# Optimization experiments

Hardware: AMD Instinct MI355X
Metric: run time of the kernel (lower is better)

## Reference

```python
import jax, jax.numpy as jnp
import numpy as np
from jax.scipy.linalg import solve_triangular

B, D, NL, NH, DH = 16, 768, 12, 12, 64
P, S, LP, NC = 10, 5, 5, 100
IMG, PATCH = 224, 16
NPTOK = (IMG // PATCH) ** 2  # 196 patches
DFF = 4 * D
LOG2PI = float(np.log(2.0 * np.pi))


def setup_inputs() -> dict:
    key = jax.random.key(0)
    ks = jax.random.split(key, 12)
    s = 0.02
    inp = {}
    inp['inputs'] = jax.random.normal(ks[0], (B, 3, IMG, IMG), jnp.float32)
    inp['patch_w'] = jax.random.normal(ks[1], (D, 3, PATCH, PATCH), jnp.float32) * s
    inp['patch_b'] = jnp.zeros((D,), jnp.float32)
    inp['cls_token'] = jax.random.normal(ks[2], (1, 1, D), jnp.float32) * s
    inp['pos_embed'] = jax.random.normal(ks[3], (1, NPTOK + 1, D), jnp.float32) * s
    inp['ln1_g'] = jnp.ones((NL, D), jnp.float32)
    inp['ln1_b'] = jnp.zeros((NL, D), jnp.float32)
    inp['qkv_w'] = jax.random.normal(ks[4], (NL, D, 3 * D), jnp.float32) * s
    inp['qkv_b'] = jnp.zeros((NL, 3 * D), jnp.float32)
    inp['proj_w'] = jax.random.normal(ks[5], (NL, D, D), jnp.float32) * s
    inp['proj_b'] = jnp.zeros((NL, D), jnp.float32)
    inp['ln2_g'] = jnp.ones((NL, D), jnp.float32)
    inp['ln2_b'] = jnp.zeros((NL, D), jnp.float32)
    inp['fc1_w'] = jax.random.normal(ks[6], (NL, D, DFF), jnp.float32) * s
    inp['fc1_b'] = jnp.zeros((NL, DFF), jnp.float32)
    inp['fc2_w'] = jax.random.normal(ks[7], (NL, DFF, D), jnp.float32) * s
    inp['fc2_b'] = jnp.zeros((NL, D), jnp.float32)
    inp['norm_g'] = jnp.ones((D,), jnp.float32)
    inp['norm_b'] = jnp.zeros((D,), jnp.float32)
    inp['head_w'] = jax.random.normal(ks[8], (D, NC), jnp.float32) * s
    inp['head_b'] = jnp.zeros((NC,), jnp.float32)
    inp['prompt'] = jax.random.normal(ks[9], (P, LP, D), jnp.float32)
    m = jax.random.normal(ks[10], (P, D), jnp.float32)
    inp['mean'] = m / jnp.linalg.norm(m, axis=-1, keepdims=True)
    # init in torch: ones + eye, repeated per pool component (positive definite)
    inp['variance'] = jnp.ones((P, D, D), jnp.float32) + jnp.eye(D, dtype=jnp.float32)[None]
    return inp


def _ln(x, g, b, eps=1e-6):
    m = x.mean(-1, keepdims=True)
    v = jnp.mean((x - m) ** 2, axis=-1, keepdims=True)
    return (x - m) * jax.lax.rsqrt(v + eps) * g + b


def _blocks(x, blk):
    def step(x, pl):
        g1, b1, qw, qb, pw, pb, g2, b2, f1w, f1b, f2w, f2b = pl
        Bn, N, _ = x.shape
        h = _ln(x, g1, b1)
        qkv = (h @ qw + qb).reshape(Bn, N, 3, NH, DH).transpose(2, 0, 3, 1, 4)
        q, k, v = qkv[0], qkv[1], qkv[2]  # [B,H,N,dh]
        att = jax.nn.softmax(jnp.einsum('bhqd,bhkd->bhqk', q, k) * (1.0 / np.sqrt(DH)), axis=-1)
        o = jnp.einsum('bhqk,bhkd->bhqd', att, v).transpose(0, 2, 1, 3).reshape(Bn, N, D)
        x = x + o @ pw + pb
        h = _ln(x, g2, b2)
        return x + jax.nn.gelu(h @ f1w + f1b) @ f2w + f2b, None
    x, _ = jax.lax.scan(step, x, blk)
    return x


def _mvn_logprob(q, mean, cov):
    # q: [B,D]; mean: [P,D]; cov: [P,D,D] -> [B,P]
    L = jnp.linalg.cholesky(cov)
    diff = q[:, None, :] - mean[None]  # [B,P,D]
    y = jax.vmap(lambda Lp, dp: solve_triangular(Lp, dp.T, lower=True), in_axes=(0, 1))(L, diff)  # [P,D,B]
    quad = jnp.sum(y * y, axis=1).T  # [B,P]
    logdet = 2.0 * jnp.sum(jnp.log(jnp.diagonal(L, axis1=-2, axis2=-1)), axis=-1)  # [P]
    return -0.5 * (D * LOG2PI + logdet[None, :] + quad)


def reference(inputs, patch_w, patch_b, cls_token, pos_embed, ln1_g, ln1_b, qkv_w, qkv_b,
              proj_w, proj_b, ln2_g, ln2_b, fc1_w, fc1_b, fc2_w, fc2_b, norm_g, norm_b,
              head_w, head_b, prompt, mean, variance):
    blk = (ln1_g, ln1_b, qkv_w, qkv_b, proj_w, proj_b, ln2_g, ln2_b, fc1_w, fc1_b, fc2_w, fc2_b)
    # patch embed: conv16x16 stride16 -> [B,196,D]
    img = jax.lax.conv_general_dilated(inputs, patch_w, (PATCH, PATCH), 'VALID',
                                       dimension_numbers=('NCHW', 'OIHW', 'NCHW'))
    img = img.reshape(B, D, NPTOK).transpose(0, 2, 1) + patch_b
    t = jnp.concatenate([jnp.broadcast_to(cls_token, (B, 1, D)), img], axis=1)
    x0 = t + pos_embed
    # query pass (no_grad in original)
    q = _ln(_blocks(x0, blk), norm_g, norm_b)[:, 0]  # [B,D]
    cov = jnp.abs(variance) + jnp.eye(D, dtype=variance.dtype)[None]
    logp = _mvn_logprob(q, mean, cov)  # [B,P]
    _, topk = jax.lax.top_k(logp, S)  # [B,S]
    prompts = prompt[topk].reshape(B, S * LP, D) + pos_embed[0, 0]
    # prompted pass: [cls(+pos), prompts, raw patch tokens]
    x = jnp.concatenate([x0[:, :1], prompts, img], axis=1)  # [B, 1+S*LP+196, D]
    x = _ln(_blocks(x, blk), norm_g, norm_b)
    x = x[:, 1:S * LP + 1].mean(axis=1)  # mean over prompt tokens
    return x @ head_w + head_b  # [B,NC]
```

## Files before the change

kernel.cpp:

```cpp
#include <hip/hip_runtime.h>
#include <stdint.h>
#include <math.h>


typedef _Float16 h16_t;
typedef _Float16 h8v __attribute__((ext_vector_type(8)));
typedef _Float16 h4v __attribute__((ext_vector_type(4)));
typedef float    f4v __attribute__((ext_vector_type(4)));

#define DEV static __device__ __forceinline__

DEV float wred64(float s) {
#pragma unroll
  for (int m = 1; m < 64; m <<= 1) s += __shfl_xor(s, m, 64);
  return s;
}
DEV float gelu_f(float x) {
  float u = 0.7978845608028654f * x * (1.0f + 0.044715f * x * x);
  u = fminf(fmaxf(u, -30.0f), 30.0f);
  float e = __expf(-2.0f * u);
  return 0.5f * x * (1.0f + (1.0f - e) / (1.0f + e));
}

#define GLD16(gp, lp) __builtin_amdgcn_global_load_lds( \
  (const __attribute__((address_space(1))) unsigned int*)(const void*)(gp), \
  (__attribute__((address_space(3))) unsigned int*)(void*)(lp), 16, 0, 0)

template <int TJ>
__global__ __launch_bounds__(256) void hgemm_t(
    const h16_t* __restrict__ A, const h16_t* __restrict__ B,
    float* __restrict__ C32, h16_t* __restrict__ C16,
    const float* __restrict__ bias,
    int M, int N, int K, int lda, int ldb, int ldc32, int ldc16,
    float alpha, int act, int addC)
{
  constexpr int BN = TJ * 32;
  __shared__ __align__(16) h16_t As[128 * 32];
  __shared__ __align__(16) h16_t Bs[BN * 32];
  int tid = threadIdx.x;
  int w = tid >> 6, lane = tid & 63;
  int m0 = blockIdx.x << 7, n0 = blockIdx.y * BN;
  int qm = (w & 1) << 6, qn = (w >> 1) * (TJ * 16);
  int scol = (lane & 3) << 3;
  int fr = lane & 15, fk = (lane >> 4) << 3;

  f4v acc[4][TJ];
#pragma unroll
  for (int i = 0; i < 4; i++)
#pragma unroll
    for (int j = 0; j < TJ; j++)
#pragma unroll
      for (int r = 0; r < 4; r++) acc[i][j][r] = 0.0f;

  for (int k0 = 0; k0 < K; k0 += 32) {
    __syncthreads();
#pragma unroll
    for (int i = 0; i < 2; i++) {
      int rr = (w << 5) + (i << 4) + (lane >> 2);
      int gm = m0 + rr; gm = gm < M ? gm : M - 1;
      GLD16(A + (size_t)gm * lda + k0 + scol, &As[((w << 5) + (i << 4)) << 5]);
    }
#pragma unroll
    for (int i = 0; i < TJ / 2; i++) {
      int rb = w * (TJ / 2) * 16 + i * 16;
      int rr = rb + (lane >> 2);
      int gn = n0 + rr; gn = gn < N ? gn : N - 1;
      GLD16(B + (size_t)gn * ldb + k0 + scol, &Bs[rb << 5]);
    }
    __syncthreads();
    h8v af[4], bf[TJ];
#pragma unroll
    for (int t = 0; t < 4; t++)
      af[t] = *(const h8v*)&As[((qm + (t << 4) + fr) << 5) + fk];
#pragma unroll
    for (int t = 0; t < TJ; t++)
      bf[t] = *(const h8v*)&Bs[((qn + (t << 4) + fr) << 5) + fk];
#pragma unroll
    for (int ti = 0; ti < 4; ti++)
#pragma unroll
      for (int tj = 0; tj < TJ; tj++)
        acc[ti][tj] = __builtin_amdgcn_mfma_f32_16x16x32_f16(af[ti], bf[tj], acc[ti][tj], 0, 0, 0);
  }

  int colb = n0 + qn + fr;
  int rowb = m0 + qm + ((lane >> 4) << 2);
#pragma unroll
  for (int tj = 0; tj < TJ; tj++) {
    int col = colb + (tj << 4);
    if (col >= N) continue;
    float bv = (bias != nullptr) ? bias[col] : 0.0f;
#pragma unroll
    for (int ti = 0; ti < 4; ti++) {
#pragma unroll
      for (int rg = 0; rg < 4; rg++) {
        int row = rowb + (ti << 4) + rg;
        if (row >= M) continue;
        float v = alpha * acc[ti][tj][rg] + bv;
        if (act) v = gelu_f(v);
        if (C32) {
          size_t off = (size_t)row * ldc32 + col;
          if (addC) v += C32[off];
          C32[off] = v;
        }
        if (C16) C16[(size_t)row * ldc16 + col] = (h16_t)v;
      }
    }
  }
}

template <int R>
DEV void stgN(const h16_t* __restrict__ src, int row0, int rowmax, int ldk,
              char* ldsb, unsigned lbase, int tid) {
#pragma unroll
  for (int r = 0; r < R; r++) {
    unsigned P = ((unsigned)r << 13) + ((unsigned)tid << 4);
    unsigned Q = P ^ (((P >> 7) & 3u) << 4);
    int row = (int)(Q >> 6);
    int kb = (int)((Q & 63u) >> 1);
    int gr = row0 + row; gr = gr < rowmax ? gr : rowmax - 1;
    GLD16(src + (size_t)gr * ldk + kb,
          ldsb + lbase + (r << 13) + ((tid >> 6) << 10));
  }
}

#define FENCE() asm volatile("" ::: "memory")
#define RBAR() do { FENCE(); __builtin_amdgcn_s_barrier(); FENCE(); } while (0)
#define VMW(N) asm volatile("s_waitcnt vmcnt(" #N ")" ::: "memory")

#define LOADFRAGS(S, G) do { \
  unsigned ab_ = cb + ((unsigned)(S) << 14); \
  unsigned bb_ = cb + 32768u + ((unsigned)(S) << 14); \
  _Pragma("unroll") for (int t = 0; t < 4; t++) { \
    unsigned PA_ = ((unsigned)((wm << 7) + ((G) << 6) + (t << 4) + fr) << 6) + ((unsigned)quad << 4); \
    PA_ ^= ((PA_ >> 7) & 3u) << 4; \
    af[t] = *(const h8v*)(ldsb + ab_ + PA_); \
    unsigned PB_ = ((unsigned)((wn << 6) + (t << 4) + fr) << 6) + ((unsigned)quad << 4); \
    PB_ ^= ((PB_ >> 7) & 3u) << 4; \
    bf[t] = *(const h8v*)(ldsb + bb_ + PB_); \
  } } while (0)

#define MM8(G) do { \
  __builtin_amdgcn_s_setprio(1); \
  _Pragma("unroll") for (int ti = 0; ti < 4; ti++) \
  _Pragma("unroll") for (int tj = 0; tj < 4; tj++) \
    acc[((G) << 2) + ti][tj] = __builtin_amdgcn_mfma_f32_16x16x32_f16(af[ti], bf[tj], acc[((G) << 2) + ti][tj], 0, 0, 0); \
  __builtin_amdgcn_s_setprio(0); } while (0)

template <int ACT>
__global__ __launch_bounds__(512, 2) void hgemm8(
    const h16_t* __restrict__ A, const h16_t* __restrict__ B,
    h16_t* __restrict__ C16, const float* __restrict__ bias,
    int M, int N, int K, int ldc16)
{
  __shared__ __align__(16) char ldsb[131072];
  int tid = threadIdx.x;
  int w = tid >> 6, lane = tid & 63;
  int wm = w >> 2, wn = w & 3;
  int fr = lane & 15, quad = lane >> 4;
  int m0 = blockIdx.x << 8, n0 = blockIdx.y << 8;

  f4v acc[8][4];
#pragma unroll
  for (int i2 = 0; i2 < 8; i2++)
#pragma unroll
    for (int j2 = 0; j2 < 4; j2++)
#pragma unroll
      for (int r2 = 0; r2 < 4; r2++) acc[i2][j2][r2] = 0.0f;

  int NT = K >> 6;

  stgN<2>(A,      m0, M, K, ldsb, 0u,              tid);
  stgN<2>(B,      n0, N, K, ldsb, 32768u,          tid);
  stgN<2>(A + 32, m0, M, K, ldsb, 16384u,          tid);
  stgN<2>(B + 32, n0, N, K, ldsb, 32768u + 16384u, tid);
  stgN<2>(A + 64, m0, M, K, ldsb, 65536u,          tid);
  stgN<2>(B + 64, n0, N, K, ldsb, 65536u + 32768u, tid);
  VMW(8);
  __builtin_amdgcn_s_barrier();
  FENCE();

  for (int i = 0; i < NT; i++) {
    unsigned cb = (unsigned)(i & 1) << 16;
    unsigned ob = cb ^ 65536u;
    int tA = (i + 1 < NT) ? i + 1 : NT - 1;
    int tB = (i + 2 < NT) ? i + 2 : NT - 1;
    h8v af[4], bf[4];

    LOADFRAGS(0, 0);
    stgN<2>(A + (tA << 6) + 32, m0, M, K, ldsb, ob + 16384u, tid);
    RBAR();
    MM8(0);
    RBAR();
    LOADFRAGS(0, 1);
    stgN<2>(B + (tA << 6) + 32, n0, N, K, ldsb, ob + 49152u, tid);
    RBAR();
    MM8(1);
    VMW(8);
    RBAR();
    LOADFRAGS(1, 0);
    stgN<2>(A + (tB << 6), m0, M, K, ldsb, cb, tid);
    RBAR();
    MM8(0);
    RBAR();
    LOADFRAGS(1, 1);
    stgN<2>(B + (tB << 6), n0, N, K, ldsb, cb + 32768u, tid);
    RBAR();
    MM8(1);
    VMW(8);
    RBAR();
  }
  asm volatile("s_waitcnt vmcnt(0)" ::: "memory");

  int row0 = m0 + (wm << 7) + (quad << 2);
  int col0 = n0 + (wn << 6) + fr;
  float bv[4];
#pragma unroll
  for (int nj = 0; nj < 4; nj++) bv[nj] = bias[col0 + (nj << 4)];
#pragma unroll
  for (int mi = 0; mi < 8; mi++) {
#pragma unroll
    for (int rg = 0; rg < 4; rg++) {
      int row = row0 + (mi << 4) + rg;
      if (row < M) {
#pragma unroll
        for (int nj = 0; nj < 4; nj++) {
          float v = acc[mi][nj][rg] + bv[nj];
          if (ACT) v = gelu_f(v);
          C16[(size_t)row * ldc16 + col0 + (nj << 4)] = (h16_t)v;
        }
      }
    }
  }
}

__global__ __launch_bounds__(512, 2) void hgemm8n(
    const h16_t* __restrict__ A, const h16_t* __restrict__ B,
    h16_t* __restrict__ C16, const float* __restrict__ bias,
    int M, int N, int K, int ldc16)
{
  __shared__ __align__(16) char ldsb[98304];
  int tid = threadIdx.x;
  int w = tid >> 6, lane = tid & 63;
  int wm = w >> 2, wn = w & 3;
  int fr = lane & 15, quad = lane >> 4;
  int m0 = blockIdx.x << 7, n0 = blockIdx.y << 8;

  f4v acc[4][4];
#pragma unroll
  for (int i2 = 0; i2 < 4; i2++)
#pragma unroll
    for (int j2 = 0; j2 < 4; j2++)
#pragma unroll
      for (int r2 = 0; r2 < 4; r2++) acc[i2][j2][r2] = 0.0f;

  int NT = K >> 6;

  stgN<1>(A,      m0, M, K, ldsb, 0u,               tid);
  stgN<2>(B,      n0, N, K, ldsb, 16384u,           tid);
  stgN<1>(A + 32, m0, M, K, ldsb, 8192u,            tid);
  stgN<2>(B + 32, n0, N, K, ldsb, 32768u,           tid);
  stgN<1>(A + 64, m0, M, K, ldsb, 49152u,           tid);
  stgN<2>(B + 64, n0, N, K, ldsb, 49152u + 16384u,  tid);
  VMW(6);
  __builtin_amdgcn_s_barrier();
  FENCE();

  for (int i = 0; i < NT; i++) {
    unsigned cb = (i & 1) ? 49152u : 0u;
    unsigned ob = cb ^ 49152u;
    int tA = (i + 1 < NT) ? i + 1 : NT - 1;
    int tB = (i + 2 < NT) ? i + 2 : NT - 1;
    h8v af[4], bf[4];

#pragma unroll
    for (int t = 0; t < 4; t++) {
      unsigned PA = ((unsigned)((wm << 6) + (t << 4) + fr) << 6) + ((unsigned)quad << 4);
      PA ^= ((PA >> 7) & 3u) << 4;
      af[t] = *(const h8v*)(ldsb + cb + PA);
      unsigned PB = ((unsigned)((wn << 6) + (t << 4) + fr) << 6) + ((unsigned)quad << 4);
      PB ^= ((PB >> 7) & 3u) << 4;
      bf[t] = *(const h8v*)(ldsb + cb + 16384u + PB);
    }
    stgN<1>(A + (tA << 6) + 32, m0, M, K, ldsb, ob + 8192u,  tid);
    stgN<2>(B + (tA << 6) + 32, n0, N, K, ldsb, ob + 32768u, tid);
    RBAR();
    __builtin_amdgcn_s_setprio(1);
#pragma unroll
    for (int ti = 0; ti < 4; ti++)
#pragma unroll
      for (int tj = 0; tj < 4; tj++)
        acc[ti][tj] = __builtin_amdgcn_mfma_f32_16x16x32_f16(af[ti], bf[tj], acc[ti][tj], 0, 0, 0);
    __builtin_amdgcn_s_setprio(0);
    VMW(6);
    RBAR();

#pragma unroll
    for (int t = 0; t < 4; t++) {
      unsigned PA = ((unsigned)((wm << 6) + (t << 4) + fr) << 6) + ((unsigned)quad << 4);
      PA ^= ((PA >> 7) & 3u) << 4;
      af[t] = *(const h8v*)(ldsb + cb + 8192u + PA);
      unsigned PB = ((unsigned)((wn << 6) + (t << 4) + fr) << 6) + ((unsigned)quad << 4);
      PB ^= ((PB >> 7) & 3u) << 4;
      bf[t] = *(const h8v*)(ldsb + cb + 32768u + PB);
    }
    stgN<1>(A + (tB << 6), m0, M, K, ldsb, cb,           tid);
    stgN<2>(B + (tB << 6), n0, N, K, ldsb, cb + 16384u,  tid);
    RBAR();
    __builtin_amdgcn_s_setprio(1);
#pragma unroll
    for (int ti = 0; ti < 4; ti++)
#pragma unroll
      for (int tj = 0; tj < 4; tj++)
        acc[ti][tj] = __builtin_amdgcn_mfma_f32_16x16x32_f16(af[ti], bf[tj], acc[ti][tj], 0, 0, 0);
    __builtin_amdgcn_s_setprio(0);
    VMW(6);
    RBAR();
  }
  asm volatile("s_waitcnt vmcnt(0)" ::: "memory");

  int row0 = m0 + (wm << 6) + (quad << 2);
  int col0 = n0 + (wn << 6) + fr;
  float bv[4];
#pragma unroll
  for (int nj = 0; nj < 4; nj++) bv[nj] = bias[col0 + (nj << 4)];
#pragma unroll
  for (int mi = 0; mi < 4; mi++) {
#pragma unroll
    for (int rg = 0; rg < 4; rg++) {
      int row = row0 + (mi << 4) + rg;
      if (row < M) {
#pragma unroll
        for (int nj = 0; nj < 4; nj++) {
          float v = acc[mi][nj][rg] + bv[nj];
          C16[(size_t)row * ldc16 + col0 + (nj << 4)] = (h16_t)v;
        }
      }
    }
  }
}

__global__ __launch_bounds__(512, 2) void hgemm128(
    const h16_t* __restrict__ A, const h16_t* __restrict__ B,
    float* __restrict__ C32, const float* __restrict__ bias,
    int M, int N, int K, int ldc, int addC)
{
  __shared__ __align__(16) char ldsb[98304];
  int tid = threadIdx.x;
  int w = tid >> 6, lane = tid & 63;
  int wm = w >> 2, wn = w & 3;
  int fr = lane & 15, quad = lane >> 4;
  int m0 = blockIdx.x << 7, n0 = blockIdx.y << 7;

  f4v acc[4][2];
#pragma unroll
  for (int i2 = 0; i2 < 4; i2++)
#pragma unroll
    for (int j2 = 0; j2 < 2; j2++)
#pragma unroll
      for (int r2 = 0; r2 < 4; r2++) acc[i2][j2][r2] = 0.0f;

  int NT = K >> 6;

  stgN<1>(A,       m0, M, K, ldsb, 0u,                tid);
  stgN<1>(A + 32,  m0, M, K, ldsb, 8192u,             tid);
  stgN<1>(B,       n0, N, K, ldsb, 16384u,            tid);
  stgN<1>(B + 32,  n0, N, K, ldsb, 24576u,            tid);
  stgN<1>(A + 64,  m0, M, K, ldsb, 32768u,            tid);
  stgN<1>(A + 96,  m0, M, K, ldsb, 32768u + 8192u,    tid);
  stgN<1>(B + 64,  n0, N, K, ldsb, 32768u + 16384u,   tid);
  stgN<1>(B + 96,  n0, N, K, ldsb, 32768u + 24576u,   tid);
  VMW(4);
  __builtin_amdgcn_s_barrier();
  FENCE();

  unsigned cb = 0u;
  unsigned sb = 65536u;
  for (int i = 0; i < NT; i++) {
    int tS = (i + 2 < NT) ? i + 2 : NT - 1;
    h8v af[2][4], bf[2][2];
#pragma unroll
    for (int kh = 0; kh < 2; kh++) {
      unsigned ab = cb + ((unsigned)kh << 13);
      unsigned bb = cb + 16384u + ((unsigned)kh << 13);
#pragma unroll
      for (int t = 0; t < 4; t++) {
        unsigned PA = ((unsigned)((wm << 6) + (t << 4) + fr) << 6) + ((unsigned)quad << 4);
        PA ^= ((PA >> 7) & 3u) << 4;
        af[kh][t] = *(const h8v*)(ldsb + ab + PA);
      }
#pragma unroll
      for (int t = 0; t < 2; t++) {
        unsigned PB = ((unsigned)((wn << 5) + (t << 4) + fr) << 6) + ((unsigned)quad << 4);
        PB ^= ((PB >> 7) & 3u) << 4;
        bf[kh][t] = *(const h8v*)(ldsb + bb + PB);
      }
    }
    stgN<1>(A + (tS << 6),      m0, M, K, ldsb, sb,           tid);
    stgN<1>(A + (tS << 6) + 32, m0, M, K, ldsb, sb + 8192u,   tid);
    stgN<1>(B + (tS << 6),      n0, N, K, ldsb, sb + 16384u,  tid);
    stgN<1>(B + (tS << 6) + 32, n0, N, K, ldsb, sb + 24576u,  tid);
    RBAR();
    __builtin_amdgcn_s_setprio(1);
#pragma unroll
    for (int kh = 0; kh < 2; kh++)
#pragma unroll
      for (int ti = 0; ti < 4; ti++)
#pragma unroll
        for (int tj = 0; tj < 2; tj++)
          acc[ti][tj] = __builtin_amdgcn_mfma_f32_16x16x32_f16(af[kh][ti], bf[kh][tj], acc[ti][tj], 0, 0, 0);
    __builtin_amdgcn_s_setprio(0);
    VMW(4);
    RBAR();
    cb = (cb == 65536u) ? 0u : cb + 32768u;
    sb = (sb == 65536u) ? 0u : sb + 32768u;
  }
  asm volatile("s_waitcnt vmcnt(0)" ::: "memory");

  int row0 = m0 + (wm << 6) + (quad << 2);
  int col0 = n0 + (wn << 5) + fr;
  float bv[2];
#pragma unroll
  for (int nj = 0; nj < 2; nj++) bv[nj] = bias[col0 + (nj << 4)];
#pragma unroll
  for (int mi = 0; mi < 4; mi++) {
#pragma unroll
    for (int rg = 0; rg < 4; rg++) {
      int row = row0 + (mi << 4) + rg;
      if (row < M) {
#pragma unroll
        for (int nj = 0; nj < 2; nj++) {
          size_t off = (size_t)row * ldc + col0 + (nj << 4);
          float v = acc[mi][nj][rg] + bv[nj];
          if (addC) v += C32[off];
          C32[off] = v;
        }
      }
    }
  }
}

__global__ __launch_bounds__(256) void flash_attn(
    const h16_t* __restrict__ qkv, h16_t* __restrict__ o, int N)
{
  int z = blockIdx.y;
  int b = z / 12, h = z - (z / 12) * 12;
  const h16_t* base = qkv + (size_t)b * N * 2304 + h * 64;
  int q0 = blockIdx.x << 6;
  int tid = threadIdx.x, w = tid >> 6, lane = tid & 63;
  int fr = lane & 15, fk = (lane >> 4) << 3;
  int quad = lane >> 4;

  __shared__ __align__(16) h16_t Qs[2][64 * 32];
  __shared__ __align__(16) h16_t Ks[2][64 * 32];
  __shared__ __align__(16) h16_t Ps[4][1024];
  __shared__ __align__(16) h16_t Vt[64 * 68];

#pragma unroll
  for (int s = 0; s < 2; s++) {
    int gq = q0 + (w << 4) + (lane >> 2); gq = gq < N ? gq : N - 1;
    GLD16(base + (size_t)gq * 2304 + (s << 5) + ((lane & 3) << 3), &Qs[s][(w << 4) << 5]);
  }
  __syncthreads();
  h8v af0 = *(const h8v*)&Qs[0][(((w << 4) + fr) << 5) + fk];
  h8v af1 = *(const h8v*)&Qs[1][(((w << 4) + fr) << 5) + fk];

  float mrow[4], lrow[4];
  f4v accO[4];
#pragma unroll
  for (int r = 0; r < 4; r++) { mrow[r] = -1e30f; lrow[r] = 0.0f; }
#pragma unroll
  for (int t = 0; t < 4; t++)
#pragma unroll
    for (int r = 0; r < 4; r++) accO[t][r] = 0.0f;

  int nj = (N + 63) >> 6;
  for (int jt = 0; jt < nj; jt++) {
    int j0 = jt << 6;
    __syncthreads();
#pragma unroll
    for (int s = 0; s < 2; s++) {
      int gj = j0 + (w << 4) + (lane >> 2); gj = gj < N ? gj : N - 1;
      GLD16(base + (size_t)gj * 2304 + 768 + (s << 5) + ((lane & 3) << 3), &Ks[s][(w << 4) << 5]);
    }
#pragma unroll
// ... 247 lines not shown
      for (int k = 0; k < c2; k++) v -= row[CB + k] * Dg[c2 * 16 + k];
      row[CB + c2] = v * Dinv[c2];
    }
  }
  __syncthreads();
}

__global__ __launch_bounds__(768) void chol_panel(float* __restrict__ Lb, int jb) {
  int p = blockIdx.x;
  float* L = Lb + (size_t)p * 589824;
  int R = 768 - jb;
  int r = threadIdx.x;
  bool actv = r < R;
  __shared__ float Bl[48 * 16];
  __shared__ float Dg[256];
  __shared__ float Dinv[16];
  float row[64];
  float* my = L + (size_t)(jb + r) * 768 + jb;
  if (actv) {
#pragma unroll
    for (int i = 0; i < 16; i++) {
      f4v v = *(const f4v*)(my + 4 * i);
      row[4 * i] = v[0]; row[4 * i + 1] = v[1]; row[4 * i + 2] = v[2]; row[4 * i + 3] = v[3];
    }
  }
  chol_sub<0>(row, r, actv, Bl, Dg, Dinv);
  chol_sub<16>(row, r, actv, Bl, Dg, Dinv);
  chol_sub<32>(row, r, actv, Bl, Dg, Dinv);
  chol_sub<48>(row, r, actv, Bl, Dg, Dinv);
  if (actv) {
#pragma unroll
    for (int i = 0; i < 16; i++) {
      f4v v; v[0] = row[4 * i]; v[1] = row[4 * i + 1]; v[2] = row[4 * i + 2]; v[3] = row[4 * i + 3];
      *(f4v*)(my + 4 * i) = v;
    }
  }
}

__global__ __launch_bounds__(256) void ltrans_k(const float* __restrict__ Lb,
                                                float* __restrict__ Ut,
                                                float* __restrict__ dg) {
  int p = blockIdx.z;
  const float* L = Lb + (size_t)p * 589824;
  float* U = Ut + (size_t)p * 589824;
  int r0 = blockIdx.x << 5, c0 = blockIdx.y << 5;
  __shared__ float t[32][33];
  int a = threadIdx.x >> 3, b4 = (threadIdx.x & 7) << 2;
  f4v v = *(const f4v*)(L + (size_t)(r0 + a) * 768 + c0 + b4);
  t[a][b4] = v[0]; t[a][b4 + 1] = v[1]; t[a][b4 + 2] = v[2]; t[a][b4 + 3] = v[3];
  __syncthreads();
  int k = c0 + a;
  f4v ov;
#pragma unroll
  for (int i = 0; i < 4; i++) {
    int j = r0 + b4 + i;
    float val = t[b4 + i][a];
    ov[i] = (j > k) ? val : 0.0f;
    if (j == k) dg[p * 768 + k] = val;
  }
  *(f4v*)(U + (size_t)k * 768 + r0 + b4) = ov;
}

__global__ __launch_bounds__(64) void trsm2(const float* __restrict__ Ut,
                                            const float* __restrict__ dg,
                                            const float* __restrict__ q,
                                            const float* __restrict__ mean,
                                            float* __restrict__ logp) {
  int gw = blockIdx.x;
  int p = gw >> 4, b = gw & 15;
  const float* U = Ut + (size_t)p * 589824;
  int lane = threadIdx.x;

  float y[12], dinv[12];
  float lacc = 0.0f;
#pragma unroll
  for (int m = 0; m < 12; m++) {
    int i = lane + (m << 6);
    y[m] = q[b * 768 + i] - mean[p * 768 + i];
    float d = dg[p * 768 + i];
    dinv[m] = 1.0f / d;
    lacc += __logf(d);
  }

  float u[4][12];
#pragma unroll
  for (int d0 = 0; d0 < 4; d0++)
#pragma unroll
    for (int mm = 0; mm < 12; mm++)
      u[d0][mm] = U[(size_t)d0 * 768 + lane + (mm << 6)];

#pragma unroll
  for (int m = 0; m < 12; m++) {
    for (int kb = 0; kb < 64; kb += 4) {
#pragma unroll
      for (int kd = 0; kd < 4; kd++) {
        int k = (m << 6) + kb + kd;
        float yo = __shfl(y[m], kb + kd, 64);
        float di = __shfl(dinv[m], kb + kd, 64);
        float yk = yo * di;
        if (lane == kb + kd) y[m] = yk;
        float un[12];
        bool pf = (k + 4) < 768;
        const float* rp = U + (size_t)(k + 4) * 768 + lane;
#pragma unroll
        for (int mm = 0; mm < 12; mm++) un[mm] = pf ? rp[mm << 6] : 0.0f;
#pragma unroll
        for (int mm = 0; mm < 12; mm++) y[mm] -= u[kd][mm] * yk;
#pragma unroll
        for (int mm = 0; mm < 12; mm++) u[kd][mm] = un[mm];
      }
    }
  }

  float quad = 0.0f;
#pragma unroll
  for (int m = 0; m < 12; m++) quad += y[m] * y[m];
  quad = wred64(quad);
  lacc = wred64(lacc);
  if (lane == 0)
    logp[b * 10 + p] = -0.5f * (768.0f * 1.8378770664093453f + 2.0f * lacc + quad);
}

__global__ void topk_k(const float* __restrict__ logp, int* __restrict__ tk) {
  int b = threadIdx.x;
  if (b >= 16) return;
  float v[10];
#pragma unroll
  for (int p = 0; p < 10; p++) v[p] = logp[b * 10 + p];
#pragma unroll
  for (int s = 0; s < 5; s++) {
    int bi = 0; float bv = v[0];
#pragma unroll
    for (int p = 1; p < 10; p++) if (v[p] > bv) { bv = v[p]; bi = p; }
    tk[b * 5 + s] = bi;
    v[bi] = -3.0e38f;
  }
}

DEV float blocksum256(float s, float* red) {
  s = wred64(s);
  __syncthreads();
  if ((threadIdx.x & 63) == 0) red[threadIdx.x >> 6] = s;
  __syncthreads();
  return red[0] + red[1] + red[2] + red[3];
}

__global__ __launch_bounds__(256) void final_head(const float* __restrict__ x,
                                                  const float* __restrict__ g,
                                                  const float* __restrict__ b,
                                                  const float* __restrict__ hw,
                                                  const float* __restrict__ hb,
                                                  float* __restrict__ out) {
  int bb = blockIdx.x, tid = threadIdx.x;
  __shared__ float xm[768];
  __shared__ float red[4];
  float a0 = 0, a1 = 0, a2 = 0;
  for (int j = 1; j <= 25; j++) {
    const float* rp = x + ((size_t)bb * 222 + j) * 768;
    float v0 = rp[tid], v1 = rp[tid + 256], v2 = rp[tid + 512];
    float s = blocksum256(v0 + v1 + v2, red);
    float mean = s * (1.0f / 768.0f);
    float d0 = v0 - mean, d1 = v1 - mean, d2 = v2 - mean;
    float s2 = blocksum256(d0 * d0 + d1 * d1 + d2 * d2, red);
    float rstd = rsqrtf(s2 * (1.0f / 768.0f) + 1e-6f);
    a0 += d0 * rstd * g[tid] + b[tid];
    a1 += d1 * rstd * g[tid + 256] + b[tid + 256];
    a2 += d2 * rstd * g[tid + 512] + b[tid + 512];
  }
  xm[tid] = a0 * (1.0f / 25.0f);
  xm[tid + 256] = a1 * (1.0f / 25.0f);
  xm[tid + 512] = a2 * (1.0f / 25.0f);
  __syncthreads();
  if (tid < 100) {
    float s = hb[tid];
    for (int d = 0; d < 768; d++) s += xm[d] * hw[d * 100 + tid];
    out[bb * 100 + tid] = s;
  }
}

extern "C" void kernel_launch(void* const* d_in, const int* in_sizes, int n_in,
                              void* d_out, int out_size, void* d_ws, size_t ws_size,
                              hipStream_t stream) {
  (void)in_sizes; (void)n_in; (void)out_size; (void)ws_size;
  const float* inp     = (const float*)d_in[0];
  const float* patchw  = (const float*)d_in[1];
  const float* patchb  = (const float*)d_in[2];
  const float* cls     = (const float*)d_in[3];
  const float* pos     = (const float*)d_in[4];
  const float* ln1g    = (const float*)d_in[5];
  const float* ln1b    = (const float*)d_in[6];
  const float* qkvw    = (const float*)d_in[7];
  const float* qkvb    = (const float*)d_in[8];
  const float* projw   = (const float*)d_in[9];
  const float* projb   = (const float*)d_in[10];
  const float* ln2g    = (const float*)d_in[11];
  const float* ln2b    = (const float*)d_in[12];
  const float* fc1w    = (const float*)d_in[13];
  const float* fc1b    = (const float*)d_in[14];
  const float* fc2w    = (const float*)d_in[15];
  const float* fc2b    = (const float*)d_in[16];
  const float* normg   = (const float*)d_in[17];
  const float* normb   = (const float*)d_in[18];
  const float* headw   = (const float*)d_in[19];
  const float* headb   = (const float*)d_in[20];
  const float* prompt  = (const float*)d_in[21];
  const float* meanp   = (const float*)d_in[22];
  const float* var     = (const float*)d_in[23];
  float* out = (float*)d_out;

  char* ws = (char*)d_ws;
  size_t cur = 0;
  auto alloc = [&](size_t bytes) { size_t r = cur; cur += (bytes + 255) & ~(size_t)255; return r; };
  float* x    = (float*)(ws + alloc((size_t)3552 * 768 * 4));
  float* img  = (float*)(ws + alloc((size_t)3136 * 768 * 4));
  float* qb   = (float*)(ws + alloc((size_t)16 * 768 * 4));
  float* logp = (float*)(ws + alloc(1024));
  int*   tk   = (int*)(ws + alloc(1024));
  float* dg   = (float*)(ws + alloc((size_t)10 * 768 * 4));
  h16_t* h16   = (h16_t*)(ws + alloc((size_t)3552 * 768 * 2));
  size_t qkv_off = alloc((size_t)3552 * 2304 * 2);
  h16_t* qkv16 = (h16_t*)(ws + qkv_off);
  size_t g_off = alloc((size_t)3552 * 3072 * 2);
  h16_t* g16   = (h16_t*)(ws + g_off);
  float* Lbuf  = (float*)(ws + alloc((size_t)10 * 589824 * 4));
  h16_t* wq16  = (h16_t*)(ws + alloc((size_t)12 * 2304 * 768 * 2));
  h16_t* wp16  = (h16_t*)(ws + alloc((size_t)12 * 768 * 768 * 2));
  h16_t* w116  = (h16_t*)(ws + alloc((size_t)12 * 3072 * 768 * 2));
  h16_t* w216  = (h16_t*)(ws + alloc((size_t)12 * 768 * 3072 * 2));
  h16_t* wpt16 = (h16_t*)(ws + alloc((size_t)768 * 768 * 2));
  h16_t* col16 = (h16_t*)(ws + g_off);
  float* Ut    = (float*)(ws + qkv_off);

  wcvt_t<<<dim3(72, 24, 12), 256, 0, stream>>>(qkvw, wq16, 768, 2304);
  wcvt_t<<<dim3(24, 24, 12), 256, 0, stream>>>(projw, wp16, 768, 768);
  wcvt_t<<<dim3(96, 24, 12), 256, 0, stream>>>(fc1w, w116, 768, 3072);
  wcvt_t<<<dim3(24, 96, 12), 256, 0, stream>>>(fc2w, w216, 3072, 768);
  cvt_flat<<<2304, 256, 0, stream>>>(patchw, wpt16, 589824);

  im2col_k<<<9408, 256, 0, stream>>>(inp, col16);
  hgemm128<<<dim3(25, 6), 512, 0, stream>>>(col16, wpt16, img, patchb,
      3136, 768, 768, 768, 0);
  build_x0_k<<<9456, 256, 0, stream>>>(x, img, cls, pos);

  auto pass = [&](int Ntok) {
    int M = 16 * Ntok;
    int Mt1 = (M + 127) / 128;
    int Mt8 = (M + 255) / 256;
    int Qt = (Ntok + 63) / 64;
    for (int l = 0; l < 12; l++) {
      ln_rows<<<(M + 3) / 4, 256, 0, stream>>>(x, h16, nullptr, ln1g + l * 768, ln1b + l * 768, M, 768, 768);
      hgemm8n<<<dim3(Mt1, 9), 512, 0, stream>>>(h16, wq16 + (size_t)l * 2304 * 768, qkv16,
          qkvb + l * 2304, M, 2304, 768, 2304);
      flash_attn<<<dim3(Qt, 192), 256, 0, stream>>>(qkv16, h16, Ntok);
      hgemm128<<<dim3(Mt1, 6), 512, 0, stream>>>(h16, wp16 + (size_t)l * 768 * 768, x,
          projb + l * 768, M, 768, 768, 768, 1);
      ln_rows<<<(M + 3) / 4, 256, 0, stream>>>(x, h16, nullptr, ln2g + l * 768, ln2b + l * 768, M, 768, 768);
      hgemm8<1><<<dim3(Mt8, 12), 512, 0, stream>>>(h16, w116 + (size_t)l * 3072 * 768, g16,
          fc1b + l * 3072, M, 3072, 768, 3072);
      hgemm128<<<dim3(Mt1, 6), 512, 0, stream>>>(g16, w216 + (size_t)l * 768 * 3072, x,
          fc2b + l * 768, M, 768, 3072, 768, 1);
    }
  };

  pass(197);
  ln_rows<<<4, 256, 0, stream>>>(x, nullptr, qb, normg, normb, 16, (long)197 * 768, 768);

  cov_init_k<<<23040, 256, 0, stream>>>(var, Lbuf);
  for (int m = 0; m < 12; m++) {
    int jb = 64 * m;
    if (m) sgemm_nt_chol<<<dim3((768 - jb) / 64, 1, 10), 256, 0, stream>>>(Lbuf, jb);
    chol_panel<<<10, 768, 0, stream>>>(Lbuf, jb);
  }
  ltrans_k<<<dim3(24, 24, 10), 256, 0, stream>>>(Lbuf, Ut, dg);
  trsm2<<<160, 64, 0, stream>>>(Ut, dg, qb, meanp, logp);
  topk_k<<<1, 64, 0, stream>>>(logp, tk);

  build_x2_k<<<10656, 256, 0, stream>>>(x, img, cls, pos, prompt, tk);
  pass(222);
  final_head<<<16, 256, 0, stream>>>(x, normg, normb, headw, headb, out);
}
```

Before: 5.356 ms.

## Restructure GEMM pipelines into triple-buffered single-barrier loops and deepen TRSM prefetch

The three MFMA GEMM kernels are rewritten around a common scheme. Each issues the next-next stage's global-to-LDS loads at the top of the iteration, then reads fragments and runs MFMAs with one barrier per K-step, rotating through three LDS buffers. The QKV GEMM grows its LDS to 144KB for triple buffering, and the FC1 kernel now steps K by 32 instead of 64. The aim is fewer barriers and better overlap of loads with compute, at the cost of more LDS and possibly lower occupancy. Separately, the TRSM kernel widens its register prefetch window from 4 to 8 rows to hide global-load latency, which raises register pressure.

```diff
diff --git a/kernel.cpp b/kernel.cpp
--- a/kernel.cpp
+++ b/kernel.cpp
@@ -25,88 +25,6 @@
 #define GLD16(gp, lp) __builtin_amdgcn_global_load_lds( \
   (const __attribute__((address_space(1))) unsigned int*)(const void*)(gp), \
   (__attribute__((address_space(3))) unsigned int*)(void*)(lp), 16, 0, 0)
-
-template <int TJ>
-__global__ __launch_bounds__(256) void hgemm_t(
-    const h16_t* __restrict__ A, const h16_t* __restrict__ B,
-    float* __restrict__ C32, h16_t* __restrict__ C16,
-    const float* __restrict__ bias,
-    int M, int N, int K, int lda, int ldb, int ldc32, int ldc16,
-    float alpha, int act, int addC)
-{
-  constexpr int BN = TJ * 32;
-  __shared__ __align__(16) h16_t As[128 * 32];
-  __shared__ __align__(16) h16_t Bs[BN * 32];
-  int tid = threadIdx.x;
-  int w = tid >> 6, lane = tid & 63;
-  int m0 = blockIdx.x << 7, n0 = blockIdx.y * BN;
-  int qm = (w & 1) << 6, qn = (w >> 1) * (TJ * 16);
-  int scol = (lane & 3) << 3;
-  int fr = lane & 15, fk = (lane >> 4) << 3;
-
-  f4v acc[4][TJ];
-#pragma unroll
-  for (int i = 0; i < 4; i++)
-#pragma unroll
-    for (int j = 0; j < TJ; j++)
-#pragma unroll
-      for (int r = 0; r < 4; r++) acc[i][j][r] = 0.0f;
-
-  for (int k0 = 0; k0 < K; k0 += 32) {
-    __syncthreads();
-#pragma unroll
-    for (int i = 0; i < 2; i++) {
-      int rr = (w << 5) + (i << 4) + (lane >> 2);
-      int gm = m0 + rr; gm = gm < M ? gm : M - 1;
-      GLD16(A + (size_t)gm * lda + k0 + scol, &As[((w << 5) + (i << 4)) << 5]);
-    }
-#pragma unroll
-    for (int i = 0; i < TJ / 2; i++) {
-      int rb = w * (TJ / 2) * 16 + i * 16;
-      int rr = rb + (lane >> 2);
-      int gn = n0 + rr; gn = gn < N ? gn : N - 1;
-      GLD16(B + (size_t)gn * ldb + k0 + scol, &Bs[rb << 5]);
-    }
-    __syncthreads();
-    h8v af[4], bf[TJ];
-#pragma unroll
-    for (int t = 0; t < 4; t++)
-      af[t] = *(const h8v*)&As[((qm + (t << 4) + fr) << 5) + fk];
-#pragma unroll
-    for (int t = 0; t < TJ; t++)
-      bf[t] = *(const h8v*)&Bs[((qn + (t << 4) + fr) << 5) + fk];
-#pragma unroll
-    for (int ti = 0; ti < 4; ti++)
-#pragma unroll
-      for (int tj = 0; tj < TJ; tj++)
-        acc[ti][tj] = __builtin_amdgcn_mfma_f32_16x16x32_f16(af[ti], bf[tj], acc[ti][tj], 0, 0, 0);
-  }
-
-  int colb = n0 + qn + fr;
-  int rowb = m0 + qm + ((lane >> 4) << 2);
-#pragma unroll
-  for (int tj = 0; tj < TJ; tj++) {
-    int col = colb + (tj << 4);
-    if (col >= N) continue;
-    float bv = (bias != nullptr) ? bias[col] : 0.0f;
-#pragma unroll
-    for (int ti = 0; ti < 4; ti++) {
-#pragma unroll
-      for (int rg = 0; rg < 4; rg++) {
-        int row = rowb + (ti << 4) + rg;
-        if (row >= M) continue;
-        float v = alpha * acc[ti][tj][rg] + bv;
-        if (act) v = gelu_f(v);
-        if (C32) {
-          size_t off = (size_t)row * ldc32 + col;
-          if (addC) v += C32[off];
-          C32[off] = v;
-        }
-        if (C16) C16[(size_t)row * ldc16 + col] = (h16_t)v;
-      }
-    }
-  }
-}
 
 template <int R>
 DEV void stgN(const h16_t* __restrict__ src, int row0, int rowmax, int ldk,
@@ -127,41 +45,27 @@
 #define RBAR() do { FENCE(); __builtin_amdgcn_s_barrier(); FENCE(); } while (0)
 #define VMW(N) asm volatile("s_waitcnt vmcnt(" #N ")" ::: "memory")
 
-#define LOADFRAGS(S, G) do { \
-  unsigned ab_ = cb + ((unsigned)(S) << 14); \
-  unsigned bb_ = cb + 32768u + ((unsigned)(S) << 14); \
-  _Pragma("unroll") for (int t = 0; t < 4; t++) { \
-    unsigned PA_ = ((unsigned)((wm << 7) + ((G) << 6) + (t << 4) + fr) << 6) + ((unsigned)quad << 4); \
-    PA_ ^= ((PA_ >> 7) & 3u) << 4; \
-    af[t] = *(const h8v*)(ldsb + ab_ + PA_); \
-    unsigned PB_ = ((unsigned)((wn << 6) + (t << 4) + fr) << 6) + ((unsigned)quad << 4); \
-    PB_ ^= ((PB_ >> 7) & 3u) << 4; \
-    bf[t] = *(const h8v*)(ldsb + bb_ + PB_); \
-  } } while (0)
-
-#define MM8(G) do { \
-  __builtin_amdgcn_s_setprio(1); \
-  _Pragma("unroll") for (int ti = 0; ti < 4; ti++) \
-  _Pragma("unroll") for (int tj = 0; tj < 4; tj++) \
-    acc[((G) << 2) + ti][tj] = __builtin_amdgcn_mfma_f32_16x16x32_f16(af[ti], bf[tj], acc[((G) << 2) + ti][tj], 0, 0, 0); \
-  __builtin_amdgcn_s_setprio(0); } while (0)
-
-template <int ACT>
-__global__ __launch_bounds__(512, 2) void hgemm8(
+DEV h8v frag_rd(const char* ldsb, unsigned rb, int row, int quad) {
+  unsigned P = ((unsigned)row << 6) + ((unsigned)quad << 4);
+  P ^= ((P >> 7) & 3u) << 4;
+  return *(const h8v*)(ldsb + rb + P);
+}
+
+__global__ __launch_bounds__(512, 2) void hgemm_q(
     const h16_t* __restrict__ A, const h16_t* __restrict__ B,
     h16_t* __restrict__ C16, const float* __restrict__ bias,
     int M, int N, int K, int ldc16)
 {
-  __shared__ __align__(16) char ldsb[131072];
+  __shared__ __align__(16) char ldsb[147456];
   int tid = threadIdx.x;
   int w = tid >> 6, lane = tid & 63;
   int wm = w >> 2, wn = w & 3;
   int fr = lane & 15, quad = lane >> 4;
-  int m0 = blockIdx.x << 8, n0 = blockIdx.y << 8;
-
-  f4v acc[8][4];
-#pragma unroll
-  for (int i2 = 0; i2 < 8; i2++)
+  int m0 = blockIdx.x << 7, n0 = blockIdx.y << 8;
+
+  f4v acc[4][4];
+#pragma unroll
+  for (int i2 = 0; i2 < 4; i2++)
 #pragma unroll
     for (int j2 = 0; j2 < 4; j2++)
 #pragma unroll
@@ -169,55 +73,55 @@
 
   int NT = K >> 6;
 
-  stgN<2>(A,      m0, M, K, ldsb, 0u,              tid);
-  stgN<2>(B,      n0, N, K, ldsb, 32768u,          tid);
-  stgN<2>(A + 32, m0, M, K, ldsb, 16384u,          tid);
-  stgN<2>(B + 32, n0, N, K, ldsb, 32768u + 16384u, tid);
-  stgN<2>(A + 64, m0, M, K, ldsb, 65536u,          tid);
-  stgN<2>(B + 64, n0, N, K, ldsb, 65536u + 32768u, tid);
-  VMW(8);
+  auto stage = [&](int t, unsigned bb) {
+    stgN<1>(A + (t << 6),      m0, M, K, ldsb, bb,           tid);
+    stgN<1>(A + (t << 6) + 32, m0, M, K, ldsb, bb + 8192u,   tid);
+    stgN<2>(B + (t << 6),      n0, N, K, ldsb, bb + 16384u,  tid);
+    stgN<2>(B + (t << 6) + 32, n0, N, K, ldsb, bb + 32768u,  tid);
+  };
+  stage(0, 0u);
+  stage(1, 49152u);
+  VMW(6);
   __builtin_amdgcn_s_barrier();
   FENCE();
 
+  unsigned cb = 0u, sb = 98304u;
   for (int i = 0; i < NT; i++) {
-    unsigned cb = (unsigned)(i & 1) << 16;
-    unsigned ob = cb ^ 65536u;
-    int tA = (i + 1 < NT) ? i + 1 : NT - 1;
-    int tB = (i + 2 < NT) ? i + 2 : NT - 1;
-    h8v af[4], bf[4];
-
-    LOADFRAGS(0, 0);
-    stgN<2>(A + (tA << 6) + 32, m0, M, K, ldsb, ob + 16384u, tid);
+    int tS = (i + 2 < NT) ? i + 2 : NT - 1;
+    stage(tS, sb);
+    h8v af[2][4], bf[2][4];
+#pragma unroll
+    for (int kh = 0; kh < 2; kh++)
+#pragma unroll
+      for (int t = 0; t < 4; t++) {
+        af[kh][t] = frag_rd(ldsb, cb + ((unsigned)kh << 13),
+                            (wm << 6) + (t << 4) + fr, quad);
+        bf[kh][t] = frag_rd(ldsb, cb + 16384u + ((unsigned)kh << 14),
+                            (wn << 6) + (t << 4) + fr, quad);
+      }
+    __builtin_amdgcn_s_setprio(1);
+#pragma unroll
+    for (int kh = 0; kh < 2; kh++)
+#pragma unroll
+      for (int ti = 0; ti < 4; ti++)
+#pragma unroll
+        for (int tj = 0; tj < 4; tj++)
+          acc[ti][tj] = __builtin_amdgcn_mfma_f32_16x16x32_f16(af[kh][ti], bf[kh][tj], acc[ti][tj], 0, 0, 0);
+    __builtin_amdgcn_s_setprio(0);
+    VMW(6);
     RBAR();
-    MM8(0);
-    RBAR();
-    LOADFRAGS(0, 1);
-    stgN<2>(B + (tA << 6) + 32, n0, N, K, ldsb, ob + 49152u, tid);
-    RBAR();
-    MM8(1);
-    VMW(8);
-    RBAR();
-    LOADFRAGS(1, 0);
-    stgN<2>(A + (tB << 6), m0, M, K, ldsb, cb, tid);
-    RBAR();
-    MM8(0);
-    RBAR();
-    LOADFRAGS(1, 1);
-    stgN<2>(B + (tB << 6), n0, N, K, ldsb, cb + 32768u, tid);
-    RBAR();
-    MM8(1);
-    VMW(8);
-    RBAR();
+    cb = (cb == 98304u) ? 0u : cb + 49152u;
+    sb = (sb == 98304u) ? 0u : sb + 49152u;
   }
   asm volatile("s_waitcnt vmcnt(0)" ::: "memory");
 
-  int row0 = m0 + (wm << 7) + (quad << 2);
+  int row0 = m0 + (wm << 6) + (quad << 2);
   int col0 = n0 + (wn << 6) + fr;
   float bv[4];
 #pragma unroll
   for (int nj = 0; nj < 4; nj++) bv[nj] = bias[col0 + (nj << 4)];
 #pragma unroll
-  for (int mi = 0; mi < 8; mi++) {
+  for (int mi = 0; mi < 4; mi++) {
 #pragma unroll
     for (int rg = 0; rg < 4; rg++) {
       int row = row0 + (mi << 4) + rg;
@@ -225,7 +129,6 @@
 #pragma unroll
         for (int nj = 0; nj < 4; nj++) {
           float v = acc[mi][nj][rg] + bv[nj];
-          if (ACT) v = gelu_f(v);
           C16[(size_t)row * ldc16 + col0 + (nj << 4)] = (h16_t)v;
         }
       }
@@ -233,7 +136,7 @@
   }
 }
 
-__global__ __launch_bounds__(512, 2) void hgemm8n(
+__global__ __launch_bounds__(512, 2) void hgemm_f(
     const h16_t* __restrict__ A, const h16_t* __restrict__ B,
     h16_t* __restrict__ C16, const float* __restrict__ bias,
     int M, int N, int K, int ldc16)
@@ -243,95 +146,67 @@
   int w = tid >> 6, lane = tid & 63;
   int wm = w >> 2, wn = w & 3;
   int fr = lane & 15, quad = lane >> 4;
-  int m0 = blockIdx.x << 7, n0 = blockIdx.y << 8;
-
-  f4v acc[4][4];
-#pragma unroll
-  for (int i2 = 0; i2 < 4; i2++)
+  int m0 = blockIdx.x << 8, n0 = blockIdx.y << 8;
+
+  f4v acc[8][4];
+#pragma unroll
+  for (int i2 = 0; i2 < 8; i2++)
 #pragma unroll
     for (int j2 = 0; j2 < 4; j2++)
 #pragma unroll
       for (int r2 = 0; r2 < 4; r2++) acc[i2][j2][r2] = 0.0f;
 
-  int NT = K >> 6;
-
-  stgN<1>(A,      m0, M, K, ldsb, 0u,               tid);
-  stgN<2>(B,      n0, N, K, ldsb, 16384u,           tid);
-  stgN<1>(A + 32, m0, M, K, ldsb, 8192u,            tid);
-  stgN<2>(B + 32, n0, N, K, ldsb, 32768u,           tid);
-  stgN<1>(A + 64, m0, M, K, ldsb, 49152u,           tid);
-  stgN<2>(B + 64, n0, N, K, ldsb, 49152u + 16384u,  tid);
-  VMW(6);
+  int NT = K >> 5;
+
+  auto stage = [&](int t, unsigned bb) {
+    stgN<2>(A + (t << 5), m0, M, K, ldsb, bb,          tid);
+    stgN<2>(B + (t << 5), n0, N, K, ldsb, bb + 16384u, tid);
+  };
+  stage(0, 0u);
+  stage(1, 32768u);
+  VMW(4);
   __builtin_amdgcn_s_barrier();
   FENCE();
 
+  unsigned cb = 0u, sb = 65536u;
   for (int i = 0; i < NT; i++) {
-    unsigned cb = (i & 1) ? 49152u : 0u;
-    unsigned ob = cb ^ 49152u;
-    int tA = (i + 1 < NT) ? i + 1 : NT - 1;
-    int tB = (i + 2 < NT) ? i + 2 : NT - 1;
-    h8v af[4], bf[4];
-
-#pragma unroll
-    for (int t = 0; t < 4; t++) {
-      unsigned PA = ((unsigned)((wm << 6) + (t << 4) + fr) << 6) + ((unsigned)quad << 4);
-      PA ^= ((PA >> 7) & 3u) << 4;
-      af[t] = *(const h8v*)(ldsb + cb + PA);
-      unsigned PB = ((unsigned)((wn << 6) + (t << 4) + fr) << 6) + ((unsigned)quad << 4);
-      PB ^= ((PB >> 7) & 3u) << 4;
-      bf[t] = *(const h8v*)(ldsb + cb + 16384u + PB);
-    }
-    stgN<1>(A + (tA << 6) + 32, m0, M, K, ldsb, ob + 8192u,  tid);
-    stgN<2>(B + (tA << 6) + 32, n0, N, K, ldsb, ob + 32768u, tid);
-    RBAR();
+    int tS = (i + 2 < NT) ? i + 2 : NT - 1;
+    stage(tS, sb);
+    h8v af[8], bf[4];
+#pragma unroll
+    for (int t = 0; t < 8; t++)
+      af[t] = frag_rd(ldsb, cb, (wm << 7) + (t << 4) + fr, quad);
+#pragma unroll
+    for (int t = 0; t < 4; t++)
+      bf[t] = frag_rd(ldsb, cb + 16384u, (wn << 6) + (t << 4) + fr, quad);
     __builtin_amdgcn_s_setprio(1);
 #pragma unroll
-    for (int ti = 0; ti < 4; ti++)
+    for (int ti = 0; ti < 8; ti++)
 #pragma unroll
       for (int tj = 0; tj < 4; tj++)
         acc[ti][tj] = __builtin_amdgcn_mfma_f32_16x16x32_f16(af[ti], bf[tj], acc[ti][tj], 0, 0, 0);
     __builtin_amdgcn_s_setprio(0);
-    VMW(6);
+    VMW(4);
     RBAR();
-
-#pragma unroll
-    for (int t = 0; t < 4; t++) {
-      unsigned PA = ((unsigned)((wm << 6) + (t << 4) + fr) << 6) + ((unsigned)quad << 4);
-      PA ^= ((PA >> 7) & 3u) << 4;
-      af[t] = *(const h8v*)(ldsb + cb + 8192u + PA);
-      unsigned PB = ((unsigned)((wn << 6) + (t << 4) + fr) << 6) + ((unsigned)quad << 4);
-      PB ^= ((PB >> 7) & 3u) << 4;
-      bf[t] = *(const h8v*)(ldsb + cb + 32768u + PB);
-    }
-    stgN<1>(A + (tB << 6), m0, M, K, ldsb, cb,           tid);
-    stgN<2>(B + (tB << 6), n0, N, K, ldsb, cb + 16384u,  tid);
-    RBAR();
-    __builtin_amdgcn_s_setprio(1);
-#pragma unroll
-    for (int ti = 0; ti < 4; ti++)
-#pragma unroll
-      for (int tj = 0; tj < 4; tj++)
-        acc[ti][tj] = __builtin_amdgcn_mfma_f32_16x16x32_f16(af[ti], bf[tj], acc[ti][tj], 0, 0, 0);
-    __builtin_amdgcn_s_setprio(0);
-    VMW(6);
-    RBAR();
+    cb = (cb == 65536u) ? 0u : cb + 32768u;
+    sb = (sb == 65536u) ? 0u : sb + 32768u;
   }
   asm volatile("s_waitcnt vmcnt(0)" ::: "memory");
 
-  int row0 = m0 + (wm << 6) + (quad << 2);
+  int row0 = m0 + (wm << 7) + (quad << 2);
   int col0 = n0 + (wn << 6) + fr;
   float bv[4];
 #pragma unroll
   for (int nj = 0; nj < 4; nj++) bv[nj] = bias[col0 + (nj << 4)];
 #pragma unroll
-  for (int mi = 0; mi < 4; mi++) {
+  for (int mi = 0; mi < 8; mi++) {
 #pragma unroll
     for (int rg = 0; rg < 4; rg++) {
       int row = row0 + (mi << 4) + rg;
       if (row < M) {
 #pragma unroll
         for (int nj = 0; nj < 4; nj++) {
-          float v = acc[mi][nj][rg] + bv[nj];
+          float v = gelu_f(acc[mi][nj][rg] + bv[nj]);
           C16[(size_t)row * ldc16 + col0 + (nj << 4)] = (h16_t)v;
         }
       }
@@ -339,7 +214,7 @@
   }
 }
 
-__global__ __launch_bounds__(512, 2) void hgemm128(
+__global__ __launch_bounds__(512, 2) void hgemm_p(
     const h16_t* __restrict__ A, const h16_t* __restrict__ B,
     float* __restrict__ C32, const float* __restrict__ bias,
     int M, int N, int K, int ldc, int addC)
@@ -361,45 +236,34 @@
 
   int NT = K >> 6;
 
-  stgN<1>(A,       m0, M, K, ldsb, 0u,                tid);
-  stgN<1>(A + 32,  m0, M, K, ldsb, 8192u,             tid);
-  stgN<1>(B,       n0, N, K, ldsb, 16384u,            tid);
-  stgN<1>(B + 32,  n0, N, K, ldsb, 24576u,            tid);
-  stgN<1>(A + 64,  m0, M, K, ldsb, 32768u,            tid);
-  stgN<1>(A + 96,  m0, M, K, ldsb, 32768u + 8192u,    tid);
-  stgN<1>(B + 64,  n0, N, K, ldsb, 32768u + 16384u,   tid);
-  stgN<1>(B + 96,  n0, N, K, ldsb, 32768u + 24576u,   tid);
+  auto stage = [&](int t, unsigned bb) {
+    stgN<1>(A + (t << 6),      m0, M, K, ldsb, bb,           tid);
+    stgN<1>(A + (t << 6) + 32, m0, M, K, ldsb, bb + 8192u,   tid);
+    stgN<1>(B + (t << 6),      n0, N, K, ldsb, bb + 16384u,  tid);
+    stgN<1>(B + (t << 6) + 32, n0, N, K, ldsb, bb + 24576u,  tid);
+  };
+  stage(0, 0u);
+  stage(1, 32768u);
   VMW(4);
   __builtin_amdgcn_s_barrier();
   FENCE();
 
-  unsigned cb = 0u;
-  unsigned sb = 65536u;
+  unsigned cb = 0u, sb = 65536u;
   for (int i = 0; i < NT; i++) {
     int tS = (i + 2 < NT) ? i + 2 : NT - 1;
+    stage(tS, sb);
     h8v af[2][4], bf[2][2];
 #pragma unroll
     for (int kh = 0; kh < 2; kh++) {
-      unsigned ab = cb + ((unsigned)kh << 13);
-      unsigned bb = cb + 16384u + ((unsigned)kh << 13);
-#pragma unroll
-      for (int t = 0; t < 4; t++) {
-        unsigned PA = ((unsigned)((wm << 6) + (t << 4) + fr) << 6) + ((unsigned)quad << 4);
-        PA ^= ((PA >> 7) & 3u) << 4;
-        af[kh][t] = *(const h8v*)(ldsb + ab + PA);
-      }
-#pragma unroll
-      for (int t = 0; t < 2; t++) {
-        unsigned PB = ((unsigned)((wn << 5) + (t << 4) + fr) << 6) + ((unsigned)quad << 4);
-        PB ^= ((PB >> 7) & 3u) << 4;
-        bf[kh][t] = *(const h8v*)(ldsb + bb + PB);
-      }
-    }
-    stgN<1>(A + (tS << 6),      m0, M, K, ldsb, sb,           tid);
-    stgN<1>(A + (tS << 6) + 32, m0, M, K, ldsb, sb + 8192u,   tid);
-    stgN<1>(B + (tS << 6),      n0, N, K, ldsb, sb + 16384u,  tid);
-    stgN<1>(B + (tS << 6) + 32, n0, N, K, ldsb, sb + 24576u,  tid);
-    RBAR();
+#pragma unroll
+      for (int t = 0; t < 4; t++)
+        af[kh][t] = frag_rd(ldsb, cb + ((unsigned)kh << 13),
+                            (wm << 6) + (t << 4) + fr, quad);
+#pragma unroll
+      for (int t = 0; t < 2; t++)
+        bf[kh][t] = frag_rd(ldsb, cb + 16384u + ((unsigned)kh << 13),
+                            (wn << 5) + (t << 4) + fr, quad);
+    }
     __builtin_amdgcn_s_setprio(1);
 #pragma unroll
     for (int kh = 0; kh < 2; kh++)
@@ -813,26 +677,26 @@
     lacc += __logf(d);
   }
 
-  float u[4][12];
-#pragma unroll
-  for (int d0 = 0; d0 < 4; d0++)
+  float u[8][12];
+#pragma unroll
+  for (int d0 = 0; d0 < 8; d0++)
 #pragma unroll
     for (int mm = 0; mm < 12; mm++)
       u[d0][mm] = U[(size_t)d0 * 768 + lane + (mm << 6)];
 
 #pragma unroll
   for (int m = 0; m < 12; m++) {
-    for (int kb = 0; kb < 64; kb += 4) {
-#pragma unroll
-      for (int kd = 0; kd < 4; kd++) {
+    for (int kb = 0; kb < 64; kb += 8) {
+#pragma unroll
+      for (int kd = 0; kd < 8; kd++) {
         int k = (m << 6) + kb + kd;
         float yo = __shfl(y[m], kb + kd, 64);
         float di = __shfl(dinv[m], kb + kd, 64);
         float yk = yo * di;
         if (lane == kb + kd) y[m] = yk;
         float un[12];
-        bool pf = (k + 4) < 768;
-        const float* rp = U + (size_t)(k + 4) * 768 + lane;
+        bool pf = (k + 8) < 768;
+        const float* rp = U + (size_t)(k + 8) * 768 + lane;
 #pragma unroll
         for (int mm = 0; mm < 12; mm++) un[mm] = pf ? rp[mm << 6] : 0.0f;
 #pragma unroll
@@ -969,7 +833,7 @@
   cvt_flat<<<2304, 256, 0, stream>>>(patchw, wpt16, 589824);
 
   im2col_k<<<9408, 256, 0, stream>>>(inp, col16);
-  hgemm128<<<dim3(25, 6), 512, 0, stream>>>(col16, wpt16, img, patchb,
+  hgemm_p<<<dim3(25, 6), 512, 0, stream>>>(col16, wpt16, img, patchb,
       3136, 768, 768, 768, 0);
   build_x0_k<<<9456, 256, 0, stream>>>(x, img, cls, pos);
 
@@ -980,15 +844,15 @@
     int Qt = (Ntok + 63) / 64;
     for (int l = 0; l < 12; l++) {
       ln_rows<<<(M + 3) / 4, 256, 0, stream>>>(x, h16, nullptr, ln1g + l * 768, ln1b + l * 768, M, 768, 768);
-      hgemm8n<<<dim3(Mt1, 9), 512, 0, stream>>>(h16, wq16 + (size_t)l * 2304 * 768, qkv16,
+      hgemm_q<<<dim3(Mt1, 9), 512, 0, stream>>>(h16, wq16 + (size_t)l * 2304 * 768, qkv16,
           qkvb + l * 2304, M, 2304, 768, 2304);
       flash_attn<<<dim3(Qt, 192), 256, 0, stream>>>(qkv16, h16, Ntok);
-      hgemm128<<<dim3(Mt1, 6), 512, 0, stream>>>(h16, wp16 + (size_t)l * 768 * 768, x,
+      hgemm_p<<<dim3(Mt1, 6), 512, 0, stream>>>(h16, wp16 + (size_t)l * 768 * 768, x,
           projb + l * 768, M, 768, 768, 768, 1);
       ln_rows<<<(M + 3) / 4, 256, 0, stream>>>(x, h16, nullptr, ln2g + l * 768, ln2b + l * 768, M, 768, 768);
-      hgemm8<1><<<dim3(Mt8, 12), 512, 0, stream>>>(h16, w116 + (size_t)l * 3072 * 768, g16,
+      hgemm_f<<<dim3(Mt8, 12), 512, 0, stream>>>(h16, w116 + (size_t)l * 3072 * 768, g16,
           fc1b + l * 3072, M, 3072, 768, 3072);
-      hgemm128<<<dim3(Mt1, 6), 512, 0, stream>>>(g16, w216 + (size_t)l * 768 * 3072, x,
+      hgemm_p<<<dim3(Mt1, 6), 512, 0, stream>>>(g16, w216 + (size_t)l * 768 * 3072, x,
           fc2b + l * 768, M, 768, 3072, 768, 1);
     }
   };
```

After: 5.333 ms. About the same (-0.4%).
